# Performance work log

Measured on AMD Instinct MI355X. Metric: run time of the kernel, lower is better.

The kernel has to match this reference:

```python
import jax, jax.numpy as jnp
import numpy as np

# Mamba2 defaults (mamba_ssm): d_state=128, d_conv=4, expand=2, headdim=64, ngroups=1
NB, D_MODEL, D_STATE, D_CONV, HEADDIM = 2, 512, 128, 4, 64
D_INNER = 2 * D_MODEL                      # expand * d_model
NHEADS = D_INNER // HEADDIM                # 16
CONV_DIM = D_INNER + 2 * D_STATE           # x, B, C go through depthwise conv
D_IN_PROJ = 2 * D_INNER + 2 * D_STATE + NHEADS  # z, xBC, dt
VOCAB, LABEL, B, L = 32000, 1000, 2, 512


def setup_inputs() -> dict:
    key = jax.random.key(0)
    ks = jax.random.split(key, 8)
    nrm = lambda k, shape, s: jax.random.normal(k, shape, dtype=jnp.float32) * s
    tokens = jax.random.randint(ks[0], (B, L), 0, VOCAB)
    embedding = nrm(ks[1], (VOCAB, D_MODEL), 0.02)
    in_proj_w = nrm(ks[2], (NB, D_IN_PROJ, D_MODEL), D_MODEL ** -0.5)
    conv_w = nrm(ks[3], (NB, CONV_DIM, D_CONV), D_CONV ** -0.5)
    conv_b = jnp.zeros((NB, CONV_DIM), jnp.float32)
    # dt_bias = inverse-softplus of dt ~ logUniform[1e-3, 0.1] (Mamba2 init)
    dt = jnp.exp(jax.random.uniform(ks[4], (NB, NHEADS), minval=float(np.log(1e-3)), maxval=float(np.log(0.1))))
    dt_bias = dt + jnp.log(-jnp.expm1(-dt))
    A_log = jnp.log(jax.random.uniform(ks[5], (NB, NHEADS), minval=1.0, maxval=16.0))
    D = jnp.ones((NB, NHEADS), jnp.float32)
    rms_w = jnp.ones((NB, D_INNER), jnp.float32)
    out_proj_w = nrm(ks[6], (NB, D_MODEL, D_INNER), D_INNER ** -0.5)
    ln_w = jnp.ones((NB, D_MODEL), jnp.float32)
    ln_b = jnp.zeros((NB, D_MODEL), jnp.float32)
    head_w = nrm(ks[7], (LABEL, D_MODEL), D_MODEL ** -0.5)
    head_b = jnp.zeros((LABEL,), jnp.float32)
    return dict(tokens=tokens, embedding=embedding, in_proj_w=in_proj_w, conv_w=conv_w,
                conv_b=conv_b, dt_bias=dt_bias, A_log=A_log, D=D, rms_w=rms_w,
                out_proj_w=out_proj_w, ln_w=ln_w, ln_b=ln_b, head_w=head_w, head_b=head_b)


def _mamba2(u, Wi, cw, cb, dtb, Alog, Dv, rw, Wo):
    b, l, _ = u.shape
    zxbcdt = u @ Wi.T                                  # (b,l,D_IN_PROJ)
    z = zxbcdt[..., :D_INNER]
    xBC = zxbcdt[..., D_INNER:D_INNER + CONV_DIM]
    dt = jax.nn.softplus(zxbcdt[..., D_INNER + CONV_DIM:] + dtb)   # (b,l,h)
    # causal depthwise conv1d, kernel size D_CONV
    xp = jnp.pad(xBC, ((0, 0), (D_CONV - 1, 0), (0, 0)))
    xBC = sum(xp[:, k:k + l, :] * cw[:, k] for k in range(D_CONV)) + cb
    xBC = jax.nn.silu(xBC)
    xh = xBC[..., :D_INNER].reshape(b, l, NHEADS, HEADDIM)
    Bm = xBC[..., D_INNER:D_INNER + D_STATE]           # (b,l,n), ngroups=1
    Cm = xBC[..., D_INNER + D_STATE:]                  # (b,l,n)
    A = -jnp.exp(Alog)                                 # (h,)
    dA = jnp.exp(dt * A)                               # (b,l,h)

    def step(h, inp):
        dA_t, dt_t, x_t, B_t, C_t = inp                # (b,h),(b,h),(b,h,p),(b,n),(b,n)
        h = h * dA_t[:, :, None, None] + (dt_t[:, :, None] * x_t)[..., None] * B_t[:, None, None, :]
        return h, jnp.einsum('bhpn,bn->bhp', h, C_t)

    h0 = jnp.zeros((b, NHEADS, HEADDIM, D_STATE), u.dtype)
    inp = (jnp.swapaxes(dA, 0, 1), jnp.swapaxes(dt, 0, 1), jnp.swapaxes(xh, 0, 1),
           jnp.swapaxes(Bm, 0, 1), jnp.swapaxes(Cm, 0, 1))
    _, ys = jax.lax.scan(step, h0, inp)
    y = jnp.swapaxes(ys, 0, 1) + Dv[:, None] * xh      # (b,l,h,p)
    # gated RMSNorm (norm_before_gate=False): normalize y*silu(z)
    y = y.reshape(b, l, D_INNER) * jax.nn.silu(z)
    y = y * jax.lax.rsqrt(jnp.mean(y * y, -1, keepdims=True) + 1e-5) * rw
    return y @ Wo.T


def _layernorm(x, w, bias):
    mu = jnp.mean(x, -1, keepdims=True)
    xc = x - mu
    var = jnp.mean(xc * xc, -1, keepdims=True)
    return xc * jax.lax.rsqrt(var + 1e-5) * w + bias


def reference(tokens, embedding, in_proj_w, conv_w, conv_b, dt_bias, A_log, D,
              rms_w, out_proj_w, ln_w, ln_b, head_w, head_b):
    x = embedding[tokens]                              # (b,l,d)
    for i in range(NB):
        y = _mamba2(x, in_proj_w[i], conv_w[i], conv_b[i], dt_bias[i],
                    A_log[i], D[i], rms_w[i], out_proj_w[i])
        x = _layernorm(y + x, ln_w[i], ln_b[i])        # residual + LN (dropout=identity)
    return x @ head_w.T + head_b                        # (b,l,label)
```

## Files before the change

kernel.cpp:

```cpp
#include <hip/hip_runtime.h>

#define L_SEQ 512
#define BATCH 2
#define NROWS (BATCH*L_SEQ)
#define DMODEL 512
#define DINNER 1024
#define DSTATE 128
#define NHEADSM 16
#define CONVD 1280
#define DINPROJ 2320
#define QCH 32
#define NCH 16
#define WI_PAD 2368
#define WH_PAD 1024

#define W_CONVW 0
#define W_CONVB 10240
#define W_DTB   12800
#define W_ALOG  12832
#define W_DD    12864
#define W_RMSW  12896
#define W_LNW   14944
#define W_LNB   15968
#define W_HEADB 16992
#define O_X     18048
#define O_ZX    (O_X  + NROWS*DMODEL)
#define O_XC    (O_ZX + NROWS*DINPROJ)
#define O_DT    (O_XC + NROWS*CONVD)
#define O_Y     (O_DT + NROWS*NHEADSM)
#define O_O     (O_Y  + NROWS*DINNER)
#define O_LA    (O_O  + NROWS*DMODEL)
#define O_S     (O_LA + 16384)
#define O_UB    (O_S  + 4194304)
#define U_WI   0
#define U_WO   2424832
#define U_WH   3473408
#define U_XBF  3997696
#define U_YBF  4521984

#define NSMALL 17992
#define NPREPW (2*WI_PAD + 2*DMODEL + WH_PAD)

typedef __attribute__((ext_vector_type(8))) short short8;
typedef __attribute__((ext_vector_type(4))) float floatx4;

__device__ __forceinline__ float b2f(unsigned short h){ return __uint_as_float(((unsigned)h)<<16); }
__device__ __forceinline__ unsigned short f2b(float x){
  unsigned u = __float_as_uint(x);
  return (unsigned short)((u + 0x7fffu + ((u>>16)&1u)) >> 16);
}
__device__ __forceinline__ float loadIn(const void* p, long i, int f){
  return f ? b2f(((const unsigned short*)p)[i]) : ((const float*)p)[i];
}

__global__ void k_detect(const unsigned* __restrict__ emb, int* __restrict__ flag){
  __shared__ int red[256];
  int t = threadIdx.x; int cnt = 0;
  for (int i = 0; i < 16; i++){
    unsigned w = emb[t*16 + i];
    unsigned e = (w >> 7) & 0xffu;
    cnt += (e >= 100 && e <= 126) ? 1 : 0;
  }
  red[t] = cnt; __syncthreads();
  if (t == 0){
    int s = 0;
    for (int i = 0; i < 256; i++) s += red[i];
    *flag = (s > 2048) ? 1 : 0;
  }
}

struct ConvArgs { const void* src[9]; int off[10]; };

__global__ void k_prep(ConvArgs a, const void* __restrict__ wi, const void* __restrict__ wo,
                       const void* __restrict__ wh, const int* __restrict__ tok,
                       const void* __restrict__ emb, const int* __restrict__ flag,
                       float* __restrict__ dstSmall,
                       unsigned short* __restrict__ WiB, unsigned short* __restrict__ WoB,
                       unsigned short* __restrict__ WhB,
                       float* __restrict__ x, unsigned short* __restrict__ xbf)
{
  int f = *flag;
  int blk = blockIdx.x;
  if (blk < 71){
    int i = blk*256 + threadIdx.x;
    if (i < a.off[9]){
      int s = 0;
      while (i >= a.off[s+1]) s++;
      dstSmall[i] = loadIn(a.src[s], i - a.off[s], f);
    }
    return;
  }
  blk -= 71;
  if (blk < NPREPW){
    int r = blk;
    const void* src = nullptr; unsigned short* dst; long sb = 0, db; int K; bool zero = false;
    if (r < 2*WI_PAD){
      int layer = r / WI_PAD, row = r % WI_PAD;
      K = DMODEL; dst = WiB; db = ((long)layer*WI_PAD + row)*DMODEL;
      if (row < DINPROJ){ src = wi; sb = ((long)layer*DINPROJ + row)*DMODEL; } else zero = true;
    } else if (r < 2*WI_PAD + 2*DMODEL){
      int rr = r - 2*WI_PAD;
      K = DINNER; dst = WoB; db = (long)rr*DINNER;
      src = wo; sb = db;
    } else {
      int row = r - 2*WI_PAD - 2*DMODEL;
      K = DMODEL; dst = WhB; db = (long)row*DMODEL;
      if (row < 1000){ src = wh; sb = db; } else zero = true;
    }
    for (int c = threadIdx.x; c < K; c += 256)
      dst[db + c] = zero ? (unsigned short)0
                         : (f ? ((const unsigned short*)src)[sb + c] : f2b(((const float*)src)[sb + c]));
    return;
  }
  int r = blk - NPREPW;
  long base = (long)tok[r] * DMODEL;
  for (int c = threadIdx.x; c < DMODEL; c += 256){
    float v = loadIn(emb, base + c, f);
    x[(long)r*DMODEL + c] = v;
    xbf[(long)r*DMODEL + c] = f ? ((const unsigned short*)emb)[base + c] : f2b(v);
  }
}

__global__ __launch_bounds__(256) void k_mfma_nt(
    const unsigned short* __restrict__ A, const unsigned short* __restrict__ B,
    void* __restrict__ C, int M, int N, int K,
    const float* __restrict__ bias, const int* __restrict__ flag, int outDual)
{
  __shared__ unsigned short As[4096];
  __shared__ unsigned short Bs[4096];
  int f = *flag;
  int t = threadIdx.x;
  int w = t >> 6, lane = t & 63;
  int quad = lane >> 4, l16 = lane & 15;
  int m0 = blockIdx.y << 6, n0 = blockIdx.x << 6;
  int wm = (w & 1) << 5, wn = (w >> 1) << 5;
  floatx4 acc[2][2];
  #pragma unroll
  for (int mi = 0; mi < 2; mi++)
    #pragma unroll
    for (int ni = 0; ni < 2; ni++) acc[mi][ni] = (floatx4){0.f,0.f,0.f,0.f};

  int idx0 = (w << 7) + lane;
  int r0s = idx0 >> 3, g0 = idx0 & 7;
  int idx1 = idx0 + 64;
  int r1s = idx1 >> 3, g1 = idx1 & 7;
  long aOff0 = (long)(m0 + r0s)*K + g0*8;
  long aOff1 = (long)(m0 + r1s)*K + g1*8;
  long bOff0 = (long)(n0 + r0s)*K + g0*8;
  long bOff1 = (long)(n0 + r1s)*K + g1*8;
  int w0 = r0s*64 + (g0 ^ (r0s & 7))*8;
  int w1 = r1s*64 + (g1 ^ (r1s & 7))*8;

  for (int k0 = 0; k0 < K; k0 += 64){
    short8 a0 = *(const short8*)&A[aOff0 + k0];
    short8 a1 = *(const short8*)&A[aOff1 + k0];
    short8 b0 = *(const short8*)&B[bOff0 + k0];
    short8 b1 = *(const short8*)&B[bOff1 + k0];
    __syncthreads();
    *(short8*)&As[w0] = a0; *(short8*)&As[w1] = a1;
    *(short8*)&Bs[w0] = b0; *(short8*)&Bs[w1] = b1;
    __syncthreads();
    #pragma unroll
    for (int ks = 0; ks < 2; ks++){
      short8 af[2], bfr[2];
      #pragma unroll
      for (int mi = 0; mi < 2; mi++){
        int r = wm + mi*16 + l16;
        int pos = ((ks << 2) + quad) ^ (r & 7);
        af[mi] = *(const short8*)&As[r*64 + pos*8];
      }
      #pragma unroll
      for (int ni = 0; ni < 2; ni++){
        int r = wn + ni*16 + l16;
        int pos = ((ks << 2) + quad) ^ (r & 7);
        bfr[ni] = *(const short8*)&Bs[r*64 + pos*8];
      }
      #pragma unroll
      for (int mi = 0; mi < 2; mi++)
        #pragma unroll
        for (int ni = 0; ni < 2; ni++)
          acc[mi][ni] = __builtin_amdgcn_mfma_f32_16x16x32_bf16(af[mi], bfr[ni], acc[mi][ni], 0, 0, 0);
    }
  }
  #pragma unroll
  for (int mi = 0; mi < 2; mi++)
    #pragma unroll
    for (int ni = 0; ni < 2; ni++){
      int col = n0 + wn + ni*16 + l16;
      if (col >= N) continue;
      float bv = bias ? bias[col] : 0.f;
      #pragma unroll
      for (int rr = 0; rr < 4; rr++){
        int row = m0 + wm + mi*16 + (quad << 2) + rr;
        float v = acc[mi][ni][rr] + bv;
        long idx = (long)row*N + col;
        if (outDual && f) ((unsigned short*)C)[idx] = f2b(v);
        else              ((float*)C)[idx] = v;
      }
    }
}

__global__ __launch_bounds__(256) void k_conv_dt(
    const float* __restrict__ zx, const float* __restrict__ cw, const float* __restrict__ cb,
    const float* __restrict__ dtb, float* __restrict__ xc, float* __restrict__ dt)
{
  int r = blockIdx.x; int b = r >> 9, l = r & 511;
  int t = threadIdx.x;
  for (int c = t; c < CONVD; c += 256){
    float s = cb[c];
    #pragma unroll
    for (int k = 0; k < 4; k++){
      int pos = l - 3 + k;
      if (pos >= 0)
        s = fmaf(zx[(long)(b*L_SEQ + pos)*DINPROJ + DINNER + c], cw[c*4 + k], s);
    }
    xc[(long)r*CONVD + c] = s / (1.f + __expf(-s));
  }
  if (t < NHEADSM){
    float v = zx[(long)r*DINPROJ + DINNER + CONVD + t] + dtb[t];
    dt[r*NHEADSM + t] = (v > 20.f) ? v : log1pf(__expf(v));
  }
}

__global__ __launch_bounds__(256) void k_chunk1(
    const float* __restrict__ xc, const float* __restrict__ dtbuf,
    const float* __restrict__ alog, const float* __restrict__ dvec,
    float* __restrict__ S, float* __restrict__ LAb, float* __restrict__ y)
{
  int c = blockIdx.x, h = blockIdx.y, b = blockIdx.z;
  int t = threadIdx.x, w = t >> 6, lane = t & 63;
  int quad = lane >> 4, l16 = lane & 15;
  int l0 = c*QCH;
  __shared__ unsigned short XT[64*40];
  __shared__ unsigned short BTc[128*40];
  __shared__ unsigned short Bb[32*136];
  __shared__ unsigned short Cb[32*136];
  __shared__ unsigned short Gb[32*40];
  __shared__ float dtl[32], lal[32], coef[32];
  float A  = -__expf(alog[h]);
  float Dv = dvec[h];

  float xv[8];
  #pragma unroll
  for (int k = 0; k < 8; k++){
    int idx = t + k*256; int j = idx >> 6, p = idx & 63;
    xv[k] = xc[(long)(b*L_SEQ + l0 + j)*CONVD + h*64 + p];
  }
  float bv[16], cv[16];
  #pragma unroll
  for (int k = 0; k < 16; k++){
    int idx = t + k*256; int j = idx >> 7, n = idx & 127;
    long rb = (long)(b*L_SEQ + l0 + j)*CONVD + DINNER;
    bv[k] = xc[rb + n];
    cv[k] = xc[rb + DSTATE + n];
  }
  if (t < 32) dtl[t] = dtbuf[(b*L_SEQ + l0 + t)*NHEADSM + h];
  __syncthreads();
  if (t == 0){ float s = 0.f; for (int i = 0; i < 32; i++){ s += dtl[i]; lal[i] = s*A; } }
  __syncthreads();
  if (t < 32){
    coef[t] = __expf(lal[31] - lal[t]) * dtl[t];
    LAb[(b*NHEADSM + h)*L_SEQ + l0 + t] = lal[t];
  }
  __syncthreads();
  #pragma unroll
  for (int k = 0; k < 8; k++){
    int idx = t + k*256; int j = idx >> 6, p = idx & 63;
    XT[p*40 + j] = f2b(xv[k]);
  }
  #pragma unroll
  for (int k = 0; k < 16; k++){
    int idx = t + k*256; int j = idx >> 7, n = idx & 127;
    Bb[j*136 + n] = f2b(bv[k]);
    Cb[j*136 + n] = f2b(cv[k]);
    BTc[n*40 + j] = f2b(bv[k] * coef[j]);
  }
  __syncthreads();

  short8 afS = *(const short8*)&XT[(w*16 + l16)*40 + quad*8];
  floatx4 accS[8];
  #pragma unroll
  for (int nb = 0; nb < 8; nb++){
    short8 bfS = *(const short8*)&BTc[(nb*16 + l16)*40 + quad*8];
    accS[nb] = __builtin_amdgcn_mfma_f32_16x16x32_bf16(afS, bfS, (floatx4){0.f,0.f,0.f,0.f}, 0, 0, 0);
  }
  int ti = w & 1, tj = w >> 1;
  floatx4 accG = (floatx4){0.f,0.f,0.f,0.f};
  #pragma unroll
  for (int ks = 0; ks < 4; ks++){
    short8 ga = *(const short8*)&Cb[(ti*16 + l16)*136 + ks*32 + quad*8];
    short8 gb = *(const short8*)&Bb[(tj*16 + l16)*136 + ks*32 + quad*8];
    accG = __builtin_amdgcn_mfma_f32_16x16x32_bf16(ga, gb, accG, 0, 0, 0);
  }
  long sb = ((long)((b*NHEADSM + h)*NCH + c))*8192;
  #pragma unroll
  for (int nb = 0; nb < 8; nb++)
    #pragma unroll
    for (int rr = 0; rr < 4; rr++)
      S[sb + (w*16 + quad*4 + rr)*128 + nb*16 + l16] = accS[nb][rr];
  #pragma unroll
  for (int rr = 0; rr < 4; rr++){
    int i = ti*16 + quad*4 + rr, j = tj*16 + l16;
    float g = (j <= i) ? __expf(lal[i] - lal[j]) * dtl[j] * accG[rr] : 0.f;
    Gb[i*40 + j] = f2b(g);
  }
  __syncthreads();
  short8 ag = *(const short8*)&Gb[(ti*16 + l16)*40 + quad*8];
  #pragma unroll
  for (int s = 0; s < 2; s++){
    int pb = (w >> 1)*2 + s;
    short8 bx = *(const short8*)&XT[(pb*16 + l16)*40 + quad*8];
    floatx4 accY = __builtin_amdgcn_mfma_f32_16x16x32_bf16(ag, bx, (floatx4){0.f,0.f,0.f,0.f}, 0, 0, 0);
    #pragma unroll
    for (int rr = 0; rr < 4; rr++){
      int i = ti*16 + quad*4 + rr, p = pb*16 + l16;
      float xval = b2f(XT[p*40 + i]);
      y[(long)(b*L_SEQ + l0 + i)*DINNER + h*64 + p] = fmaf(Dv, xval, accY[rr]);
    }
  }
}

__global__ __launch_bounds__(256) void k_chunk2(
    float* __restrict__ S, const float* __restrict__ LAb)
{
  int bh = blockIdx.x >> 5;
  int e = ((blockIdx.x & 31) << 8) + threadIdx.x;
  long base = (long)bh*NCH*8192 + e;
  int laBase = bh*L_SEQ;
  float lam[NCH];
  #pragma unroll
  for (int c = 0; c < NCH; c++) lam[c] = __expf(LAb[laBase + c*QCH + QCH - 1]);
  float hr = 0.f;
  #pragma unroll
  for (int c = 0; c < NCH; c++){
    long off = base + (long)c*8192;
    float sv = S[off];
    S[off] = hr;
    hr = fmaf(hr, lam[c], sv);
  }
}

__global__ __launch_bounds__(256) void k_chunk3(
    const float* __restrict__ xc, const float* __restrict__ H,
    const float* __restrict__ LAb, float* __restrict__ y)
{
  int c = blockIdx.x, h = blockIdx.y, b = blockIdx.z;
  int t = threadIdx.x, w = t >> 6, lane = t & 63;
  int quad = lane >> 4, l16 = lane & 15;
  int l0 = c*QCH;
  __shared__ unsigned short Cb[32*136];
  __shared__ unsigned short Hhi[64*136];
  __shared__ unsigned short Hlo[64*136];
  __shared__ float el[32];
  if (t < 32) el[t] = __expf(LAb[(b*NHEADSM + h)*L_SEQ + l0 + t]);
  #pragma unroll
  for (int k = 0; k < 16; k++){
    int idx = t + k*256; int j = idx >> 7, n = idx & 127;
    Cb[j*136 + n] = f2b(xc[(long)(b*L_SEQ + l0 + j)*CONVD + DINNER + DSTATE + n]);
  }
  long hb = ((long)((b*NHEADSM + h)*NCH + c))*8192;
  #pragma unroll
  for (int k = 0; k < 32; k++){
    int idx = t + k*256; int p = idx >> 7, n = idx & 127;
    float v = H[hb + idx];
    unsigned short hi = f2b(v);
    Hhi[p*136 + n] = hi;
    Hlo[p*136 + n] = f2b(v - b2f(hi));
  }
  __syncthreads();
  int ti = w & 1;
  #pragma unroll
  for (int s = 0; s < 2; s++){
    int pb = (w >> 1)*2 + s;
    floatx4 acc = (floatx4){0.f,0.f,0.f,0.f};
    #pragma unroll
    for (int ks = 0; ks < 4; ks++){
      short8 a  = *(const short8*)&Cb [(ti*16 + l16)*136 + ks*32 + quad*8];
      short8 bl = *(const short8*)&Hlo[(pb*16 + l16)*136 + ks*32 + quad*8];
      short8 bh = *(const short8*)&Hhi[(pb*16 + l16)*136 + ks*32 + quad*8];
      acc = __builtin_amdgcn_mfma_f32_16x16x32_bf16(a, bl, acc, 0, 0, 0);
      acc = __builtin_amdgcn_mfma_f32_16x16x32_bf16(a, bh, acc, 0, 0, 0);
    }
    #pragma unroll
    for (int rr = 0; rr < 4; rr++){
      int i = ti*16 + quad*4 + rr, p = pb*16 + l16;
      long yb = (long)(b*L_SEQ + l0 + i)*DINNER + h*64 + p;
      y[yb] = fmaf(el[i], acc[rr], y[yb]);
    }
  }
}

__global__ __launch_bounds__(256) void k_gated_rms(
    const float* __restrict__ y, const float* __restrict__ zx, const float* __restrict__ rw,
    unsigned short* __restrict__ ybf)
{
  int r = blockIdx.x, t = threadIdx.x;
  float g[4]; float ss = 0.f;
  #pragma unroll
  for (int i = 0; i < 4; i++){
    int c = t + i*256;
    float z  = zx[(long)r*DINPROJ + c];
    float yv = y[(long)r*DINNER + c];
    float gz = z / (1.f + __expf(-z));
    g[i] = yv * gz;
    ss = fmaf(g[i], g[i], ss);
  }
  #pragma unroll
  for (int o = 1; o < 64; o <<= 1) ss += __shfl_xor(ss, o);
  __shared__ float red[4];
  int w = t >> 6, lane = t & 63;
  if (lane == 0) red[w] = ss;
  __syncthreads();
  float tot = red[0] + red[1] + red[2] + red[3];
  float sc = rsqrtf(tot / (float)DINNER + 1e-5f);
  #pragma unroll
  for (int i = 0; i < 4; i++){
    int c = t + i*256;
    ybf[(long)r*DINNER + c] = f2b(g[i] * sc * rw[c]);
  }
}

__global__ __launch_bounds__(256) void k_add_ln(
    float* __restrict__ x, const float* __restrict__ o,
    const float* __restrict__ lw, const float* __restrict__ lb,
    unsigned short* __restrict__ xbf)
{
  int r = blockIdx.x, t = threadIdx.x;
  float v[2]; float sm = 0.f;
  #pragma unroll
  for (int i = 0; i < 2; i++){ int c = t + i*256; v[i] = x[(long)r*DMODEL + c] + o[(long)r*DMODEL + c]; sm += v[i]; }
  #pragma unroll
  for (int off = 1; off < 64; off <<= 1) sm += __shfl_xor(sm, off);
  __shared__ float red[4]; __shared__ float red2[4];
  int w = t >> 6, lane = t & 63;
  if (lane == 0) red[w] = sm;
  __syncthreads();
  float mu = (red[0] + red[1] + red[2] + red[3]) / (float)DMODEL;
  float var = 0.f;
  #pragma unroll
  for (int i = 0; i < 2; i++){ v[i] -= mu; var = fmaf(v[i], v[i], var); }
  #pragma unroll
  for (int off = 1; off < 64; off <<= 1) var += __shfl_xor(var, off);
  if (lane == 0) red2[w] = var;
  __syncthreads();
  float vv = (red2[0] + red2[1] + red2[2] + red2[3]) / (float)DMODEL;
  float sc = rsqrtf(vv + 1e-5f);
  #pragma unroll
  for (int i = 0; i < 2; i++){
    int c = t + i*256;
    float ov = v[i]*sc*lw[c] + lb[c];
    x[(long)r*DMODEL + c] = ov;
    xbf[(long)r*DMODEL + c] = f2b(ov);
  }
}

extern "C" void kernel_launch(void* const* d_in, const int* in_sizes, int n_in,
                              void* d_out, int out_size, void* d_ws, size_t ws_size,
                              hipStream_t stream)
{
  const int* tokens = (const int*)d_in[0];
  const void* emb = d_in[1];
  int* flag = (int*)d_ws;
  float* ws = (float*)((char*)d_ws + 256);

  k_detect<<<1, 256, 0, stream>>>((const unsigned*)emb, flag);

  ConvArgs ca;
  const int sizes[9] = {10240, 2560, 32, 32, 32, 2048, 1024, 1024, 1000};
  const int idxs[9]  = {3, 4, 5, 6, 7, 8, 10, 11, 13};
  int off = 0;
  for (int s = 0; s < 9; s++){ ca.src[s] = d_in[idxs[s]]; ca.off[s] = off; off += sizes[s]; }
  ca.off[9] = off;

  float* X  = ws + O_X;
  float* ZX = ws + O_ZX;
  float* XC = ws + O_XC;
  float* DT = ws + O_DT;
  float* Y  = ws + O_Y;
  float* Ob = ws + O_O;
  float* LA = ws + O_LA;
  float* Sb = ws + O_S;
  unsigned short* ub  = (unsigned short*)(ws + O_UB);
  unsigned short* WiB = ub + U_WI;
  unsigned short* WoB = ub + U_WO;
  unsigned short* WhB = ub + U_WH;
  unsigned short* Xbf = ub + U_XBF;
  unsigned short* Ybf = ub + U_YBF;

  k_prep<<<71 + NPREPW + NROWS, 256, 0, stream>>>(
      ca, d_in[2], d_in[9], d_in[12], tokens, emb, flag,
      ws, WiB, WoB, WhB, X, Xbf);

  for (int layer = 0; layer < 2; layer++){
    k_mfma_nt<<<dim3(WI_PAD/64, NROWS/64), 256, 0, stream>>>(
        Xbf, WiB + (long)layer*WI_PAD*DMODEL, (void*)ZX,
        NROWS, DINPROJ, DMODEL, (const float*)nullptr, flag, 0);
    k_conv_dt<<<NROWS, 256, 0, stream>>>(
        ZX, ws + W_CONVW + layer*5120, ws + W_CONVB + layer*1280, ws + W_DTB + layer*16, XC, DT);
    k_chunk1<<<dim3(NCH, NHEADSM, BATCH), 256, 0, stream>>>(
        XC, DT, ws + W_ALOG + layer*16, ws + W_DD + layer*16, Sb, LA, Y);
    k_chunk2<<<1024, 256, 0, stream>>>(Sb, LA);
    k_chunk3<<<dim3(NCH, NHEADSM, BATCH), 256, 0, stream>>>(XC, Sb, LA, Y);
    k_gated_rms<<<NROWS, 256, 0, stream>>>(Y, ZX, ws + W_RMSW + layer*1024, Ybf);
    k_mfma_nt<<<dim3(DMODEL/64, NROWS/64), 256, 0, stream>>>(
        Ybf, WoB + (long)layer*DMODEL*DINNER, (void*)Ob,
        NROWS, DMODEL, DINNER, (const float*)nullptr, flag, 0);
    k_add_ln<<<NROWS, 256, 0, stream>>>(X, Ob, ws + W_LNW + layer*512, ws + W_LNB + layer*512, Xbf);
  }

  k_mfma_nt<<<dim3(WH_PAD/64, NROWS/64), 256, 0, stream>>>(
      Xbf, WhB, d_out, NROWS, 1000, DMODEL, ws + W_HEADB, flag, 1);
}
```

Baseline: 255.8 us.

## Double-buffer GEMM with direct global-to-LDS loads, templated tiles, and warp-shuffle scan

The bf16 MFMA GEMM now uses global_load_lds to copy tiles straight into LDS, double-buffered so the next K tile loads while the current one is computed. Tile sizes become template parameters, and the smaller out-projection and head GEMMs get 32-row tiles to launch more blocks. The chunk kernel's serial single-thread prefix sum over dt is replaced by a warp shuffle scan, which also removes two barriers. The cost is double the LDS per block and a dependence on the swizzled direct-to-LDS copy matching the fragment read layout.

```diff
diff --git a/kernel.cpp b/kernel.cpp
--- a/kernel.cpp
+++ b/kernel.cpp
@@ -53,6 +53,11 @@
   return f ? b2f(((const unsigned short*)p)[i]) : ((const float*)p)[i];
 }
 
+__device__ __forceinline__ void gload16(const void* g, void* l){
+  __builtin_amdgcn_global_load_lds((const __attribute__((address_space(1))) void*)g,
+                                   (__attribute__((address_space(3))) void*)l, 16, 0, 0);
+}
+
 __global__ void k_detect(const unsigned* __restrict__ emb, int* __restrict__ flag){
   __shared__ int red[256];
   int t = threadIdx.x; int cnt = 0;
@@ -121,71 +126,96 @@
   }
 }
 
+template<int BM, int BN>
 __global__ __launch_bounds__(256) void k_mfma_nt(
     const unsigned short* __restrict__ A, const unsigned short* __restrict__ B,
     void* __restrict__ C, int M, int N, int K,
     const float* __restrict__ bias, const int* __restrict__ flag, int outDual)
 {
-  __shared__ unsigned short As[4096];
-  __shared__ unsigned short Bs[4096];
+  constexpr int MI = BM/32;
+  constexpr int NI = BN/32;
+  constexpr int CA = BM/32;
+  constexpr int CB = BN/32;
+  __shared__ __align__(16) unsigned short As[2][BM*64];
+  __shared__ __align__(16) unsigned short Bs[2][BN*64];
   int f = *flag;
   int t = threadIdx.x;
   int w = t >> 6, lane = t & 63;
   int quad = lane >> 4, l16 = lane & 15;
-  int m0 = blockIdx.y << 6, n0 = blockIdx.x << 6;
-  int wm = (w & 1) << 5, wn = (w >> 1) << 5;
-  floatx4 acc[2][2];
-  #pragma unroll
-  for (int mi = 0; mi < 2; mi++)
-    #pragma unroll
-    for (int ni = 0; ni < 2; ni++) acc[mi][ni] = (floatx4){0.f,0.f,0.f,0.f};
-
-  int idx0 = (w << 7) + lane;
-  int r0s = idx0 >> 3, g0 = idx0 & 7;
-  int idx1 = idx0 + 64;
-  int r1s = idx1 >> 3, g1 = idx1 & 7;
-  long aOff0 = (long)(m0 + r0s)*K + g0*8;
-  long aOff1 = (long)(m0 + r1s)*K + g1*8;
-  long bOff0 = (long)(n0 + r0s)*K + g0*8;
-  long bOff1 = (long)(n0 + r1s)*K + g1*8;
-  int w0 = r0s*64 + (g0 ^ (r0s & 7))*8;
-  int w1 = r1s*64 + (g1 ^ (r1s & 7))*8;
-
-  for (int k0 = 0; k0 < K; k0 += 64){
-    short8 a0 = *(const short8*)&A[aOff0 + k0];
-    short8 a1 = *(const short8*)&A[aOff1 + k0];
-    short8 b0 = *(const short8*)&B[bOff0 + k0];
-    short8 b1 = *(const short8*)&B[bOff1 + k0];
-    __syncthreads();
-    *(short8*)&As[w0] = a0; *(short8*)&As[w1] = a1;
-    *(short8*)&Bs[w0] = b0; *(short8*)&Bs[w1] = b1;
-    __syncthreads();
+  int m0 = blockIdx.y * BM, n0 = blockIdx.x * BN;
+  int wm = (w & 1) * (BM/2), wn = (w >> 1) * (BN/2);
+  floatx4 acc[MI][NI];
+  #pragma unroll
+  for (int mi = 0; mi < MI; mi++)
+    #pragma unroll
+    for (int ni = 0; ni < NI; ni++) acc[mi][ni] = (floatx4){0.f,0.f,0.f,0.f};
+
+  const char* Ag = (const char*)A;
+  const char* Bg = (const char*)B;
+  long aOff[CA]; int aL[CA];
+  #pragma unroll
+  for (int j = 0; j < CA; j++){
+    int i = (w*CA + j)*64 + lane;
+    int r = i >> 3, g = (i & 7) ^ (r & 7);
+    aOff[j] = ((long)(m0 + r)*K + g*8)*2;
+    aL[j] = (w*CA + j)*1024;
+  }
+  long bOff[CB]; int bL[CB];
+  #pragma unroll
+  for (int j = 0; j < CB; j++){
+    int i = (w*CB + j)*64 + lane;
+    int r = i >> 3, g = (i & 7) ^ (r & 7);
+    bOff[j] = ((long)(n0 + r)*K + g*8)*2;
+    bL[j] = (w*CB + j)*1024;
+  }
+
+  const int NKI = K >> 6;
+  #pragma unroll
+  for (int j = 0; j < CA; j++) gload16(Ag + aOff[j], (char*)As[0] + aL[j]);
+  #pragma unroll
+  for (int j = 0; j < CB; j++) gload16(Bg + bOff[j], (char*)Bs[0] + bL[j]);
+  asm volatile("s_waitcnt vmcnt(0)" ::: "memory");
+  __syncthreads();
+
+  for (int ki = 0; ki < NKI; ki++){
+    int cur = ki & 1;
+    if (ki + 1 < NKI){
+      long kb = (long)(ki + 1)*128;
+      #pragma unroll
+      for (int j = 0; j < CA; j++) gload16(Ag + aOff[j] + kb, (char*)As[cur^1] + aL[j]);
+      #pragma unroll
+      for (int j = 0; j < CB; j++) gload16(Bg + bOff[j] + kb, (char*)Bs[cur^1] + bL[j]);
+    }
+    const unsigned short* Ac = As[cur];
+    const unsigned short* Bc = Bs[cur];
     #pragma unroll
     for (int ks = 0; ks < 2; ks++){
-      short8 af[2], bfr[2];
+      short8 af[MI], bfr[NI];
       #pragma unroll
-      for (int mi = 0; mi < 2; mi++){
+      for (int mi = 0; mi < MI; mi++){
         int r = wm + mi*16 + l16;
         int pos = ((ks << 2) + quad) ^ (r & 7);
-        af[mi] = *(const short8*)&As[r*64 + pos*8];
+        af[mi] = *(const short8*)&Ac[r*64 + pos*8];
       }
       #pragma unroll
-      for (int ni = 0; ni < 2; ni++){
+      for (int ni = 0; ni < NI; ni++){
         int r = wn + ni*16 + l16;
         int pos = ((ks << 2) + quad) ^ (r & 7);
-        bfr[ni] = *(const short8*)&Bs[r*64 + pos*8];
+        bfr[ni] = *(const short8*)&Bc[r*64 + pos*8];
       }
       #pragma unroll
-      for (int mi = 0; mi < 2; mi++)
+      for (int mi = 0; mi < MI; mi++)
         #pragma unroll
-        for (int ni = 0; ni < 2; ni++)
+        for (int ni = 0; ni < NI; ni++)
           acc[mi][ni] = __builtin_amdgcn_mfma_f32_16x16x32_bf16(af[mi], bfr[ni], acc[mi][ni], 0, 0, 0);
     }
-  }
-  #pragma unroll
-  for (int mi = 0; mi < 2; mi++)
-    #pragma unroll
-    for (int ni = 0; ni < 2; ni++){
+    asm volatile("s_waitcnt vmcnt(0)" ::: "memory");
+    __syncthreads();
+  }
+  #pragma unroll
+  for (int mi = 0; mi < MI; mi++)
+    #pragma unroll
+    for (int ni = 0; ni < NI; ni++){
       int col = n0 + wn + ni*16 + l16;
       if (col >= N) continue;
       float bv = bias ? bias[col] : 0.f;
@@ -254,13 +284,20 @@
     bv[k] = xc[rb + n];
     cv[k] = xc[rb + DSTATE + n];
   }
-  if (t < 32) dtl[t] = dtbuf[(b*L_SEQ + l0 + t)*NHEADSM + h];
-  __syncthreads();
-  if (t == 0){ float s = 0.f; for (int i = 0; i < 32; i++){ s += dtl[i]; lal[i] = s*A; } }
-  __syncthreads();
   if (t < 32){
-    coef[t] = __expf(lal[31] - lal[t]) * dtl[t];
-    LAb[(b*NHEADSM + h)*L_SEQ + l0 + t] = lal[t];
+    float d = dtbuf[(b*L_SEQ + l0 + t)*NHEADSM + h];
+    dtl[t] = d;
+    float s = d;
+    #pragma unroll
+    for (int o = 1; o < 32; o <<= 1){
+      float u = __shfl_up(s, o, 32);
+      if (t >= o) s += u;
+    }
+    float la = s * A;
+    lal[t] = la;
+    float tot = __shfl(s, 31, 32) * A;
+    coef[t] = __expf(tot - la) * d;
+    LAb[(b*NHEADSM + h)*L_SEQ + l0 + t] = la;
   }
   __syncthreads();
   #pragma unroll
@@ -492,7 +529,7 @@
       ws, WiB, WoB, WhB, X, Xbf);
 
   for (int layer = 0; layer < 2; layer++){
-    k_mfma_nt<<<dim3(WI_PAD/64, NROWS/64), 256, 0, stream>>>(
+    k_mfma_nt<64,64><<<dim3(WI_PAD/64, NROWS/64), 256, 0, stream>>>(
         Xbf, WiB + (long)layer*WI_PAD*DMODEL, (void*)ZX,
         NROWS, DINPROJ, DMODEL, (const float*)nullptr, flag, 0);
     k_conv_dt<<<NROWS, 256, 0, stream>>>(
@@ -502,12 +539,12 @@
     k_chunk2<<<1024, 256, 0, stream>>>(Sb, LA);
     k_chunk3<<<dim3(NCH, NHEADSM, BATCH), 256, 0, stream>>>(XC, Sb, LA, Y);
     k_gated_rms<<<NROWS, 256, 0, stream>>>(Y, ZX, ws + W_RMSW + layer*1024, Ybf);
-    k_mfma_nt<<<dim3(DMODEL/64, NROWS/64), 256, 0, stream>>>(
+    k_mfma_nt<32,32><<<dim3(DMODEL/32, NROWS/32), 256, 0, stream>>>(
         Ybf, WoB + (long)layer*DMODEL*DINNER, (void*)Ob,
         NROWS, DMODEL, DINNER, (const float*)nullptr, flag, 0);
     k_add_ln<<<NROWS, 256, 0, stream>>>(X, Ob, ws + W_LNW + layer*512, ws + W_LNB + layer*512, Xbf);
   }
 
-  k_mfma_nt<<<dim3(WH_PAD/64, NROWS/64), 256, 0, stream>>>(
+  k_mfma_nt<32,64><<<dim3(WH_PAD/64, NROWS/32), 256, 0, stream>>>(
       Xbf, WhB, d_out, NROWS, 1000, DMODEL, ws + W_HEADB, flag, 1);
 }
```

After: 249.7 us. 1.02x faster.
